# Kernel tuning notes

Hardware: AMD Instinct MI355X
Metric: run time of the kernel (lower is better)

## Reference

```python
import jax, jax.numpy as jnp
import numpy as np

N_NODES = 50000
N_EDGES = 800000
D_IN = 128
HIDDEN = [128, 128]
D_OUT = 64


def setup_inputs() -> dict:
    key = jax.random.key(0)
    ks = jax.random.split(key, 12)
    x = jax.random.normal(ks[0], (N_NODES, D_IN), dtype=jnp.float32)
    edge_index = jax.random.randint(ks[1], (2, N_EDGES), 0, N_NODES, dtype=jnp.int64)
    # SAGEConv params: lin_l acts on aggregated neighbors (has bias), lin_r on root
    def lin(k, fan_in, fan_out):
        s = 1.0 / np.sqrt(fan_in)
        return jax.random.uniform(k, (fan_in, fan_out), jnp.float32, -s, s)
    dims = [D_IN] + HIDDEN
    inp = {"x": x, "edge_index": edge_index}
    for i in range(len(HIDDEN)):
        inp[f"Wl{i}"] = lin(ks[2 + 3 * i], dims[i], dims[i + 1])
        inp[f"Wr{i}"] = lin(ks[3 + 3 * i], dims[i], dims[i + 1])
        inp[f"b{i}"] = jnp.zeros((dims[i + 1],), jnp.float32)
    inp["Wfc"] = lin(ks[10], HIDDEN[-1], D_OUT)
    inp["bfc"] = jnp.zeros((D_OUT,), jnp.float32)
    return inp


def _sage_conv(x, src, dst, n, Wl, Wr, b, deg_inv):
    # mean-aggregate source features into destination nodes
    agg = jax.ops.segment_sum(x[src], dst, num_segments=n) * deg_inv[:, None]
    return agg @ Wl + x @ Wr + b


def reference(x, edge_index, Wl0, Wr0, b0, Wl1, Wr1, b1, Wfc, bfc):
    src, dst = edge_index[0], edge_index[1]
    n = x.shape[0]
    deg = jax.ops.segment_sum(jnp.ones((src.shape[0],), x.dtype), dst, num_segments=n)
    deg_inv = 1.0 / jnp.maximum(deg, 1.0)
    h = jax.nn.relu(_sage_conv(x, src, dst, n, Wl0, Wr0, b0, deg_inv))
    # dropout p=0 / eval mode -> identity
    h = jax.nn.relu(_sage_conv(h, src, dst, n, Wl1, Wr1, b1, deg_inv))
    return h @ Wfc + bfc
```

## Files before the change

### kernel.cpp

```cpp
#include <hip/hip_runtime.h>
#include <hip/hip_bf16.h>

#define NN 50000
#define NE 800000
#define D 128
#define DOUT 64
#define PAD 64
#define BSH 8
#define NBUCK 196
#define CHUNK 4096
#define NBINB 196
#define SEGC 64
#define BPITCH 68
#define EPITCH 72
#define N8 (NN * D / 8)

typedef __attribute__((ext_vector_type(8))) short short8;
typedef __attribute__((ext_vector_type(4))) float float4v;


__device__ inline unsigned short f2bf(float f) {
    union { float f; unsigned int i; } c; c.f = f;
    unsigned int u = c.i;
    return (unsigned short)((u + 0x7fffu + ((u >> 16) & 1u)) >> 16);
}
__device__ inline float bflo(unsigned int u) {
    union { unsigned int i; float f; } c; c.i = u << 16; return c.f;
}
__device__ inline float bfhi(unsigned int u) {
    union { unsigned int i; float f; } c; c.i = u & 0xffff0000u; return c.f;
}


struct Stage1Args {
    const int* src;
    const int* dst;
    unsigned int* binned;
    int* cnts;
    const float* W[5];
    unsigned short* P[5];
    const float* x;
    unsigned short* xb;
    unsigned short* zrow;
};

__global__ void stage1(Stage1Args args) {
    int blk = blockIdx.x;
    int tid = threadIdx.x;
    if (blk < NBINB) {
        __shared__ int cnt[NBUCK];
        __shared__ __align__(16) unsigned int buf[NBUCK * BPITCH];
        for (int b = tid; b < NBUCK; b += 256) cnt[b] = 0;
        __syncthreads();
        int base = blk * CHUNK;
#pragma unroll
        for (int i = 0; i < 16; ++i) {
            int e = base + i * 256 + tid;
            if (e < NE) {
                unsigned int d = (unsigned int)args.dst[e];
                unsigned int s = (unsigned int)args.src[e];
                int q = d >> BSH;
                int slot = atomicAdd(&cnt[q], 1);
                if (slot < SEGC)
                    buf[q * BPITCH + slot] = (d << 16) | s;
            }
        }
        __syncthreads();
        for (int b = tid; b < NBUCK; b += 256)
            args.cnts[blk * NBUCK + b] = (cnt[b] < SEGC) ? cnt[b] : SEGC;
        uint4* ob = (uint4*)(args.binned + (size_t)blk * NBUCK * SEGC);
        for (int j = tid; j < NBUCK * (SEGC / 4); j += 256) {
            int q2 = j >> 4;
            int part = j & 15;
            ob[j] = *(const uint4*)&buf[q2 * BPITCH + part * 4];
        }
    } else {
        int b = blk - NBINB;
        if (b < 36) {
            int idx = b * 256 + tid;
            const float* W;
            unsigned short* P;
            int COLS, local;
            if (idx < 4 * 2048) {
                int wsel = idx >> 11;
                W = args.W[wsel]; P = args.P[wsel]; COLS = 128; local = idx & 2047;
            } else {
                W = args.W[4]; P = args.P[4]; COLS = 64; local = idx - 4 * 2048;
            }
            int CT = COLS >> 4;
            int lane = local & 63;
            int fi = local >> 6;
            int ct = fi % CT;
            int kstep = fi / CT;
            int krow = kstep * 32 + (lane >> 4) * 8;
            int col = ct * 16 + (lane & 15);
            unsigned short v[8];
#pragma unroll
            for (int j = 0; j < 8; ++j) v[j] = f2bf(W[(size_t)(krow + j) * COLS + col]);
            unsigned int w0 = v[0] | ((unsigned int)v[1] << 16);
            unsigned int w1 = v[2] | ((unsigned int)v[3] << 16);
            unsigned int w2 = v[4] | ((unsigned int)v[5] << 16);
            unsigned int w3 = v[6] | ((unsigned int)v[7] << 16);
            *(uint4*)(P + (size_t)local * 8) = make_uint4(w0, w1, w2, w3);
            if (b == 0 && tid < 16)
                *(uint4*)(args.zrow + (size_t)tid * 8) = make_uint4(0, 0, 0, 0);
        } else {
            int stride = (gridDim.x - NBINB - 36) * 256;
            for (int i = (b - 36) * 256 + tid; i < N8; i += stride) {
                const float4* p = (const float4*)args.x + (size_t)i * 2;
                float4 a = p[0], bb = p[1];
                unsigned int w0 = f2bf(a.x) | ((unsigned int)f2bf(a.y) << 16);
                unsigned int w1 = f2bf(a.z) | ((unsigned int)f2bf(a.w) << 16);
                unsigned int w2 = f2bf(bb.x) | ((unsigned int)f2bf(bb.y) << 16);
                unsigned int w3 = f2bf(bb.z) | ((unsigned int)f2bf(bb.w) << 16);
                *(uint4*)(args.xb + (size_t)i * 8) = make_uint4(w0, w1, w2, w3);
            }
        }
    }
}


__global__ __launch_bounds__(1024)
void scatter_bucket(const unsigned int* __restrict__ binned, const int* __restrict__ cnts,
                    unsigned short* __restrict__ eidx_pad, int* __restrict__ cursor) {
    __shared__ int cur[256];
    __shared__ int segc[NBINB];
    __shared__ __align__(16) unsigned short eix[256 * EPITCH];
    int q = blockIdx.x;
    int tid = threadIdx.x;
    if (tid < 256) cur[tid] = 0;
    for (int s = tid; s < NBINB; s += 1024) segc[s] = cnts[(size_t)s * NBUCK + q];
    __syncthreads();
    for (int i4 = tid; i4 < NBINB * (SEGC / 4); i4 += 1024) {
        int seg = i4 >> 4;
        int kb = (i4 & 15) << 2;
        uint4 r4 = *(const uint4*)(binned + ((size_t)seg * NBUCK + q) * SEGC + kb);
        int c = segc[seg];
#define PLACE(rv, ok)                                                     \
        if (ok) {                                                         \
            int dl = ((rv) >> 16) & 255;                                  \
            int sl = atomicAdd(&cur[dl], 1);                              \
            if (sl < PAD) eix[dl * EPITCH + sl] = (unsigned short)((rv) & 0xffffu); \
        }
        PLACE(r4.x, kb + 0 < c)
        PLACE(r4.y, kb + 1 < c)
        PLACE(r4.z, kb + 2 < c)
        PLACE(r4.w, kb + 3 < c)
#undef PLACE
    }
    __syncthreads();
    int nbase = q << BSH;
    int nlim = NN - nbase;
    if (nlim > 256) nlim = 256;
    uint4* op = (uint4*)(eidx_pad + (size_t)nbase * PAD);
    for (int j = tid; j < 2048; j += 1024) {
        int node = j >> 3;
        if (node < nlim)
            op[j] = *(const uint4*)&eix[node * EPITCH + (j & 7) * 8];
    }
    if (tid < 256) {
        int node = nbase + tid;
        if (node < NN) cursor[node] = (cur[tid] < PAD) ? cur[tid] : PAD;
    }
}


template <bool FUSEFC>
__global__ __launch_bounds__(256, 4)
void fused_layer(const unsigned short* __restrict__ feat,
                 const int* __restrict__ cursor, const unsigned short* __restrict__ eidx_pad,
                 const unsigned short* __restrict__ zrow,
                 const unsigned short* __restrict__ Pl, const unsigned short* __restrict__ Pr,
                 const float* __restrict__ bias,
                 const unsigned short* __restrict__ Pfc, const float* __restrict__ bfc,
                 unsigned short* __restrict__ outb, float* __restrict__ outf, int n) {
    __shared__ __align__(16) unsigned short As[64][136];

    int tid = threadIdx.x;
    int row0 = blockIdx.x * 64;

    {
        int g = tid >> 4;
        int l = tid & 15;
        int nbase = row0 + g * 4;
        int4 dv = *(const int4*)(cursor + nbase);
        const unsigned short* rbase = eidx_pad + (size_t)nbase * PAD;
        uint4 ia = *(const uint4*)(rbase);
        uint4 ib = *(const uint4*)(rbase + 8);
#pragma unroll
        for (int nn = 0; nn < 4; ++nn) {
            int r = g * 4 + nn;
            int node = nbase + nn;
            uint4 ca = ia, cb = ib;
            if (nn < 3) {
                ia = *(const uint4*)(rbase + (nn + 1) * PAD);
                ib = *(const uint4*)(rbase + (nn + 1) * PAD + 8);
            }
            int deg = 0;
            if (node < n) {
                deg = ((const int*)&dv)[nn];
                if (deg > PAD) deg = PAD;
            }
            float di = 1.0f / (float)(deg > 1 ? deg : 1);
            float acc[8] = {0.f, 0.f, 0.f, 0.f, 0.f, 0.f, 0.f, 0.f};
            {
                int id[16];
                id[0] = ca.x & 0xffff;  id[1] = ca.x >> 16;
                id[2] = ca.y & 0xffff;  id[3] = ca.y >> 16;
                id[4] = ca.z & 0xffff;  id[5] = ca.z >> 16;
                id[6] = ca.w & 0xffff;  id[7] = ca.w >> 16;
                id[8] = cb.x & 0xffff;  id[9] = cb.x >> 16;
                id[10] = cb.y & 0xffff; id[11] = cb.y >> 16;
                id[12] = cb.z & 0xffff; id[13] = cb.z >> 16;
                id[14] = cb.w & 0xffff; id[15] = cb.w >> 16;
                uint4 v[16];
#pragma unroll
                for (int k = 0; k < 16; ++k) {
                    const unsigned short* sp = (k < deg) ? (feat + (size_t)id[k] * D) : zrow;
                    v[k] = *(const uint4*)(sp + l * 8);
                }
#pragma unroll
                for (int k = 0; k < 16; ++k) {
                    acc[0] += bflo(v[k].x); acc[1] += bfhi(v[k].x);
                    acc[2] += bflo(v[k].y); acc[3] += bfhi(v[k].y);
                    acc[4] += bflo(v[k].z); acc[5] += bfhi(v[k].z);
                    acc[6] += bflo(v[k].w); acc[7] += bfhi(v[k].w);
                }
                const unsigned short* rowp = rbase + nn * PAD;
                int p = 16;
                while (p < deg) {
                    uint4 iv = *(const uint4*)(rowp + p);
                    int jd[8];
                    jd[0] = iv.x & 0xffff; jd[1] = iv.x >> 16;
                    jd[2] = iv.y & 0xffff; jd[3] = iv.y >> 16;
                    jd[4] = iv.z & 0xffff; jd[5] = iv.z >> 16;
                    jd[6] = iv.w & 0xffff; jd[7] = iv.w >> 16;
                    uint4 w[8];
#pragma unroll
                    for (int k = 0; k < 8; ++k) {
                        const unsigned short* sp = (p + k < deg) ? (feat + (size_t)jd[k] * D) : zrow;
                        w[k] = *(const uint4*)(sp + l * 8);
                    }
#pragma unroll
                    for (int k = 0; k < 8; ++k) {
                        acc[0] += bflo(w[k].x); acc[1] += bfhi(w[k].x);
                        acc[2] += bflo(w[k].y); acc[3] += bfhi(w[k].y);
                        acc[4] += bflo(w[k].z); acc[5] += bfhi(w[k].z);
                        acc[6] += bflo(w[k].w); acc[7] += bfhi(w[k].w);
                    }
                    p += 8;
                }
            }
            unsigned int w0 = f2bf(acc[0] * di) | ((unsigned int)f2bf(acc[1] * di) << 16);
            unsigned int w1 = f2bf(acc[2] * di) | ((unsigned int)f2bf(acc[3] * di) << 16);
            unsigned int w2 = f2bf(acc[4] * di) | ((unsigned int)f2bf(acc[5] * di) << 16);
            unsigned int w3 = f2bf(acc[6] * di) | ((unsigned int)f2bf(acc[7] * di) << 16);
            *(uint4*)&As[r][l * 8] = make_uint4(w0, w1, w2, w3);
        }
    }

    int wave = tid >> 6;
    int lane = tid & 63;
    int m16 = lane & 15;
    int quad = lane >> 4;
    int rt0 = (wave & 1) * 32;
    int ctb = (wave >> 1) * 4;

    float4v acc[2][4];
#pragma unroll
    for (int t = 0; t < 2; ++t)
#pragma unroll
        for (int c = 0; c < 4; ++c) acc[t][c] = (float4v){0.f, 0.f, 0.f, 0.f};

#pragma unroll
    for (int ks = 0; ks < 4; ++ks) {
        short8 xf[2];
#pragma unroll
        for (int t = 0; t < 2; ++t) {
            int row = row0 + rt0 + t * 16 + m16;
            short8 z = {0, 0, 0, 0, 0, 0, 0, 0};
            xf[t] = (row < n) ? *(const short8*)(feat + (size_t)row * D + ks * 32 + quad * 8) : z;
        }
#pragma unroll
        for (int c = 0; c < 4; ++c) {
            short8 bf = *(const short8*)(Pr + ((size_t)((ks * 8 + ctb + c) * 64 + lane)) * 8);
#pragma unroll
            for (int t = 0; t < 2; ++t)
                acc[t][c] = __builtin_amdgcn_mfma_f32_16x16x32_bf16(xf[t], bf, acc[t][c], 0, 0, 0);
        }
    }

    __syncthreads();

#pragma unroll
    for (int ks = 0; ks < 4; ++ks) {
        short8 af[2];
#pragma unroll
        for (int t = 0; t < 2; ++t)
            af[t] = *(const short8*)&As[rt0 + t * 16 + m16][ks * 32 + quad * 8];
#pragma unroll
        for (int c = 0; c < 4; ++c) {
            short8 bf = *(const short8*)(Pl + ((size_t)((ks * 8 + ctb + c) * 64 + lane)) * 8);
#pragma unroll
            for (int t = 0; t < 2; ++t)
                acc[t][c] = __builtin_amdgcn_mfma_f32_16x16x32_bf16(af[t], bf, acc[t][c], 0, 0, 0);
        }
    }

    if (!FUSEFC) {
#pragma unroll
        for (int t = 0; t < 2; ++t) {
#pragma unroll
            for (int c = 0; c < 4; ++c) {
                int col = (ctb + c) * 16 + m16;
                float bv = bias[col];
#pragma unroll
                for (int i = 0; i < 4; ++i) {
                    int row = row0 + rt0 + t * 16 + quad * 4 + i;
                    if (row < n)
                        outb[(size_t)row * D + col] = f2bf(fmaxf(acc[t][c][i] + bv, 0.f));
                }
            }
        }
    } else {
        __syncthreads();
#pragma unroll
        for (int t = 0; t < 2; ++t) {
#pragma unroll
            for (int c = 0; c < 4; ++c) {
                int col = (ctb + c) * 16 + m16;
                float bv = bias[col];
#pragma unroll
                for (int i = 0; i < 4; ++i) {
                    int row = rt0 + t * 16 + quad * 4 + i;
                    As[row][col] = f2bf(fmaxf(acc[t][c][i] + bv, 0.f));
                }
            }
        }
        __syncthreads();

        int ctbF = (wave >> 1) * 2;
        float4v acc2[2][2];
#pragma unroll
        for (int t = 0; t < 2; ++t)
#pragma unroll
            for (int c = 0; c < 2; ++c) acc2[t][c] = (float4v){0.f, 0.f, 0.f, 0.f};
#pragma unroll
        for (int ks = 0; ks < 4; ++ks) {
            short8 hf[2];
#pragma unroll
            for (int t = 0; t < 2; ++t)
                hf[t] = *(const short8*)&As[rt0 + t * 16 + m16][ks * 32 + quad * 8];
#pragma unroll
            for (int c = 0; c < 2; ++c) {
                short8 bf = *(const short8*)(Pfc + ((size_t)((ks * 4 + ctbF + c) * 64 + lane)) * 8);
#pragma unroll
                for (int t = 0; t < 2; ++t)
                    acc2[t][c] = __builtin_amdgcn_mfma_f32_16x16x32_bf16(hf[t], bf, acc2[t][c], 0, 0, 0);
            }
        }
#pragma unroll
        for (int t = 0; t < 2; ++t) {
#pragma unroll
            for (int c = 0; c < 2; ++c) {
                int col = (ctbF + c) * 16 + m16;
                float bv = bfc[col];
#pragma unroll
                for (int i = 0; i < 4; ++i) {
                    int row = row0 + rt0 + t * 16 + quad * 4 + i;
                    if (row < n)
                        outf[(size_t)row * DOUT + col] = acc2[t][c][i] + bv;
                }
            }
        }
    }
}


extern "C" void kernel_launch(void* const* d_in, const int* in_sizes, int n_in,
                              void* d_out, int out_size, void* d_ws, size_t ws_size,
                              hipStream_t stream) {
    const float* x   = (const float*)d_in[0];
    const int*   ei  = (const int*)d_in[1];
    const float* Wl0 = (const float*)d_in[2];
    const float* Wr0 = (const float*)d_in[3];
    const float* b0  = (const float*)d_in[4];
    const float* Wl1 = (const float*)d_in[5];
    const float* Wr1 = (const float*)d_in[6];
    const float* b1  = (const float*)d_in[7];
    const float* Wfc = (const float*)d_in[8];
    const float* bfc = (const float*)d_in[9];
    float* out = (float*)d_out;

    const int* src = ei;
    const int* dst = ei + NE;

    char* p = (char*)d_ws;
    auto carve = [&](size_t bytes) {
        char* q = p;
        p += (bytes + 255) & ~(size_t)255;
        return q;
    };
    int*            cursor   = (int*)carve(NN * sizeof(int));
    int*            cnts     = (int*)carve((size_t)NBINB * NBUCK * sizeof(int));
    unsigned short* zrow     = (unsigned short*)carve(256);
    unsigned int*   binned   = (unsigned int*)carve((size_t)NBINB * NBUCK * SEGC * 4);
    unsigned short* eidx_pad = (unsigned short*)carve((size_t)NN * PAD * 2);
    unsigned short* xb   = (unsigned short*)carve((size_t)NN * D * 2);
    unsigned short* h0b  = (unsigned short*)carve((size_t)NN * D * 2);
    unsigned short* Wl0p = (unsigned short*)carve(D * D * 2);
    unsigned short* Wr0p = (unsigned short*)carve(D * D * 2);
    unsigned short* Wl1p = (unsigned short*)carve(D * D * 2);
    unsigned short* Wr1p = (unsigned short*)carve(D * D * 2);
    unsigned short* Wfcp = (unsigned short*)carve(D * DOUT * 2);

    Stage1Args sa;
    sa.src = src; sa.dst = dst;
    sa.binned = binned; sa.cnts = cnts;
    sa.W[0] = Wl0; sa.W[1] = Wr0; sa.W[2] = Wl1; sa.W[3] = Wr1; sa.W[4] = Wfc;
    sa.P[0] = Wl0p; sa.P[1] = Wr0p; sa.P[2] = Wl1p; sa.P[3] = Wr1p; sa.P[4] = Wfcp;
    sa.x = x; sa.xb = xb; sa.zrow = zrow;
    stage1<<<NBINB + 256, 256, 0, stream>>>(sa);

    scatter_bucket<<<NBUCK, 1024, 0, stream>>>(binned, cnts, eidx_pad, cursor);

    const int GB = (NN + 63) / 64;

    fused_layer<false><<<GB, 256, 0, stream>>>(xb, cursor, eidx_pad, zrow, Wl0p, Wr0p, b0,
                                               nullptr, nullptr, h0b, nullptr, NN);
    fused_layer<true><<<GB, 256, 0, stream>>>(h0b, cursor, eidx_pad, zrow, Wl1p, Wr1p, b1,
                                              Wfcp, bfc, nullptr, out, NN);
}
```

Before: 179.4 us.

## Move weight packing and input cast from binning kernel into scatter kernel

```diff
diff --git a/kernel.cpp b/kernel.cpp
--- a/kernel.cpp
+++ b/kernel.cpp
@@ -15,6 +15,9 @@
 #define EPITCH 72
 #define N8 (NN * D / 8)
 
+#define PACKB2 9
+#define CASTB2 128
+
 typedef __attribute__((ext_vector_type(8))) short short8;
 typedef __attribute__((ext_vector_type(4))) float float4v;
 
@@ -32,11 +35,46 @@
 }
 
 
-struct Stage1Args {
-    const int* src;
-    const int* dst;
-    unsigned int* binned;
-    int* cnts;
+__global__ void bin_edges(const int* __restrict__ src, const int* __restrict__ dst,
+                          unsigned int* __restrict__ binned, int* __restrict__ cnts) {
+    __shared__ int cnt[NBUCK];
+    __shared__ __align__(16) unsigned int buf[NBUCK * BPITCH];
+    int blk = blockIdx.x;
+    int tid = threadIdx.x;
+    for (int b = tid; b < NBUCK; b += 256) cnt[b] = 0;
+    __syncthreads();
+    int base = blk * CHUNK;
+#pragma unroll
+    for (int i = 0; i < 16; ++i) {
+        int e = base + i * 256 + tid;
+        if (e < NE) {
+            unsigned int d = (unsigned int)dst[e];
+            unsigned int s = (unsigned int)src[e];
+            int q = d >> BSH;
+            int slot = atomicAdd(&cnt[q], 1);
+            if (slot < SEGC)
+                buf[q * BPITCH + slot] = (d << 16) | s;
+        }
+    }
+    __syncthreads();
+    for (int b = tid; b < NBUCK; b += 256)
+        cnts[blk * NBUCK + b] = (cnt[b] < SEGC) ? cnt[b] : SEGC;
+    uint4* ob = (uint4*)(binned + (size_t)blk * NBUCK * SEGC);
+    for (int j = tid; j < NBUCK * (SEGC / 4); j += 256) {
+        int q2 = j >> 4;
+        int part = j & 15;
+        int c = cnt[q2] < SEGC ? cnt[q2] : SEGC;
+        if (part * 4 < c)
+            ob[j] = *(const uint4*)&buf[q2 * BPITCH + part * 4];
+    }
+}
+
+
+struct Stage2Args {
+    const unsigned int* binned;
+    const int* cnts;
+    unsigned short* eidx_pad;
+    int* cursor;
     const float* W[5];
     unsigned short* P[5];
     const float* x;
@@ -44,40 +82,54 @@
     unsigned short* zrow;
 };
 
-__global__ void stage1(Stage1Args args) {
+__global__ __launch_bounds__(1024)
+void stage2(Stage2Args args) {
     int blk = blockIdx.x;
     int tid = threadIdx.x;
-    if (blk < NBINB) {
-        __shared__ int cnt[NBUCK];
-        __shared__ __align__(16) unsigned int buf[NBUCK * BPITCH];
-        for (int b = tid; b < NBUCK; b += 256) cnt[b] = 0;
+    if (blk < NBUCK) {
+        __shared__ int cur[256];
+        __shared__ int segc[NBINB];
+        __shared__ __align__(16) unsigned short eix[256 * EPITCH];
+        int q = blk;
+        if (tid < 256) cur[tid] = 0;
+        for (int s = tid; s < NBINB; s += 1024) segc[s] = args.cnts[(size_t)s * NBUCK + q];
         __syncthreads();
-        int base = blk * CHUNK;
-#pragma unroll
-        for (int i = 0; i < 16; ++i) {
-            int e = base + i * 256 + tid;
-            if (e < NE) {
-                unsigned int d = (unsigned int)args.dst[e];
-                unsigned int s = (unsigned int)args.src[e];
-                int q = d >> BSH;
-                int slot = atomicAdd(&cnt[q], 1);
-                if (slot < SEGC)
-                    buf[q * BPITCH + slot] = (d << 16) | s;
+        for (int i4 = tid; i4 < NBINB * (SEGC / 4); i4 += 1024) {
+            int seg = i4 >> 4;
+            int kb = (i4 & 15) << 2;
+            int c = segc[seg];
+            if (kb < c) {
+                uint4 r4 = *(const uint4*)(args.binned + ((size_t)seg * NBUCK + q) * SEGC + kb);
+#define PLACE(rv, ok)                                                     \
+                if (ok) {                                                 \
+                    int dl = ((rv) >> 16) & 255;                          \
+                    int sl = atomicAdd(&cur[dl], 1);                      \
+                    if (sl < PAD) eix[dl * EPITCH + sl] = (unsigned short)((rv) & 0xffffu); \
+                }
+                PLACE(r4.x, true)
+                PLACE(r4.y, kb + 1 < c)
+                PLACE(r4.z, kb + 2 < c)
+                PLACE(r4.w, kb + 3 < c)
+#undef PLACE
             }
         }
         __syncthreads();
-        for (int b = tid; b < NBUCK; b += 256)
-            args.cnts[blk * NBUCK + b] = (cnt[b] < SEGC) ? cnt[b] : SEGC;
-        uint4* ob = (uint4*)(args.binned + (size_t)blk * NBUCK * SEGC);
-        for (int j = tid; j < NBUCK * (SEGC / 4); j += 256) {
-            int q2 = j >> 4;
-            int part = j & 15;
-            ob[j] = *(const uint4*)&buf[q2 * BPITCH + part * 4];
-        }
-    } else {
-        int b = blk - NBINB;
-        if (b < 36) {
-            int idx = b * 256 + tid;
+        int nbase = q << BSH;
+        int nlim = NN - nbase;
+        if (nlim > 256) nlim = 256;
+        uint4* op = (uint4*)(args.eidx_pad + (size_t)nbase * PAD);
+        for (int j = tid; j < 2048; j += 1024) {
+            int node = j >> 3;
+            if (node < nlim)
+                op[j] = *(const uint4*)&eix[node * EPITCH + (j & 7) * 8];
+        }
+        if (tid < 256) {
+            int node = nbase + tid;
+            if (node < NN) args.cursor[node] = (cur[tid] < PAD) ? cur[tid] : PAD;
+        }
+    } else if (blk < NBUCK + PACKB2) {
+        int idx = (blk - NBUCK) * 1024 + tid;
+        if (idx < 9216) {
             const float* W;
             unsigned short* P;
             int COLS, local;
@@ -102,65 +154,20 @@
             unsigned int w2 = v[4] | ((unsigned int)v[5] << 16);
             unsigned int w3 = v[6] | ((unsigned int)v[7] << 16);
             *(uint4*)(P + (size_t)local * 8) = make_uint4(w0, w1, w2, w3);
-            if (b == 0 && tid < 16)
-                *(uint4*)(args.zrow + (size_t)tid * 8) = make_uint4(0, 0, 0, 0);
-        } else {
-            int stride = (gridDim.x - NBINB - 36) * 256;
-            for (int i = (b - 36) * 256 + tid; i < N8; i += stride) {
-                const float4* p = (const float4*)args.x + (size_t)i * 2;
-                float4 a = p[0], bb = p[1];
-                unsigned int w0 = f2bf(a.x) | ((unsigned int)f2bf(a.y) << 16);
-                unsigned int w1 = f2bf(a.z) | ((unsigned int)f2bf(a.w) << 16);
-                unsigned int w2 = f2bf(bb.x) | ((unsigned int)f2bf(bb.y) << 16);
-                unsigned int w3 = f2bf(bb.z) | ((unsigned int)f2bf(bb.w) << 16);
-                *(uint4*)(args.xb + (size_t)i * 8) = make_uint4(w0, w1, w2, w3);
-            }
-        }
-    }
-}
-
-
-__global__ __launch_bounds__(1024)
-void scatter_bucket(const unsigned int* __restrict__ binned, const int* __restrict__ cnts,
-                    unsigned short* __restrict__ eidx_pad, int* __restrict__ cursor) {
-    __shared__ int cur[256];
-    __shared__ int segc[NBINB];
-    __shared__ __align__(16) unsigned short eix[256 * EPITCH];
-    int q = blockIdx.x;
-    int tid = threadIdx.x;
-    if (tid < 256) cur[tid] = 0;
-    for (int s = tid; s < NBINB; s += 1024) segc[s] = cnts[(size_t)s * NBUCK + q];
-    __syncthreads();
-    for (int i4 = tid; i4 < NBINB * (SEGC / 4); i4 += 1024) {
-        int seg = i4 >> 4;
-        int kb = (i4 & 15) << 2;
-        uint4 r4 = *(const uint4*)(binned + ((size_t)seg * NBUCK + q) * SEGC + kb);
-        int c = segc[seg];
-#define PLACE(rv, ok)                                                     \
-        if (ok) {                                                         \
-            int dl = ((rv) >> 16) & 255;                                  \
-            int sl = atomicAdd(&cur[dl], 1);                              \
-            if (sl < PAD) eix[dl * EPITCH + sl] = (unsigned short)((rv) & 0xffffu); \
-        }
-        PLACE(r4.x, kb + 0 < c)
-        PLACE(r4.y, kb + 1 < c)
-        PLACE(r4.z, kb + 2 < c)
-        PLACE(r4.w, kb + 3 < c)
-#undef PLACE
-    }
-    __syncthreads();
-    int nbase = q << BSH;
-    int nlim = NN - nbase;
-    if (nlim > 256) nlim = 256;
-    uint4* op = (uint4*)(eidx_pad + (size_t)nbase * PAD);
-    for (int j = tid; j < 2048; j += 1024) {
-        int node = j >> 3;
-        if (node < nlim)
-            op[j] = *(const uint4*)&eix[node * EPITCH + (j & 7) * 8];
-    }
-    if (tid < 256) {
-        int node = nbase + tid;
-        if (node < NN) cursor[node] = (cur[tid] < PAD) ? cur[tid] : PAD;
+        }
+        if (blk == NBUCK && tid < 16)
+            *(uint4*)(args.zrow + (size_t)tid * 8) = make_uint4(0, 0, 0, 0);
+    } else {
+        int stride = CASTB2 * 1024;
+        for (int i = (blk - NBUCK - PACKB2) * 1024 + tid; i < N8; i += stride) {
+            const float4* p = (const float4*)args.x + (size_t)i * 2;
+            float4 a = p[0], bb = p[1];
+            unsigned int w0 = f2bf(a.x) | ((unsigned int)f2bf(a.y) << 16);
+            unsigned int w1 = f2bf(a.z) | ((unsigned int)f2bf(a.w) << 16);
+            unsigned int w2 = f2bf(bb.x) | ((unsigned int)f2bf(bb.y) << 16);
+            unsigned int w3 = f2bf(bb.z) | ((unsigned int)f2bf(bb.w) << 16);
+            *(uint4*)(args.xb + (size_t)i * 8) = make_uint4(w0, w1, w2, w3);
+        }
     }
 }
 
@@ -414,15 +421,15 @@
     unsigned short* Wr1p = (unsigned short*)carve(D * D * 2);
     unsigned short* Wfcp = (unsigned short*)carve(D * DOUT * 2);
 
-    Stage1Args sa;
-    sa.src = src; sa.dst = dst;
-    sa.binned = binned; sa.cnts = cnts;
-    sa.W[0] = Wl0; sa.W[1] = Wr0; sa.W[2] = Wl1; sa.W[3] = Wr1; sa.W[4] = Wfc;
-    sa.P[0] = Wl0p; sa.P[1] = Wr0p; sa.P[2] = Wl1p; sa.P[3] = Wr1p; sa.P[4] = Wfcp;
-    sa.x = x; sa.xb = xb; sa.zrow = zrow;
-    stage1<<<NBINB + 256, 256, 0, stream>>>(sa);
-
-    scatter_bucket<<<NBUCK, 1024, 0, stream>>>(binned, cnts, eidx_pad, cursor);
+    bin_edges<<<NBINB, 256, 0, stream>>>(src, dst, binned, cnts);
+
+    Stage2Args s2;
+    s2.binned = binned; s2.cnts = cnts;
+    s2.eidx_pad = eidx_pad; s2.cursor = cursor;
+    s2.W[0] = Wl0; s2.W[1] = Wr0; s2.W[2] = Wl1; s2.W[3] = Wr1; s2.W[4] = Wfc;
+    s2.P[0] = Wl0p; s2.P[1] = Wr0p; s2.P[2] = Wl1p; s2.P[3] = Wr1p; s2.P[4] = Wfcp;
+    s2.x = x; s2.xb = xb; s2.zrow = zrow;
+    stage2<<<NBUCK + PACKB2 + CASTB2, 1024, 0, stream>>>(s2);
 
     const int GB = (NN + 63) / 64;
 
```

Measured after the change: 183.4 us. 2.2% more time.
